# Kernel optimization log

Measured on AMD Instinct MI355X. Metric: run time of the kernel, lower is better.

The kernel has to match this reference:

```python
import jax, jax.numpy as jnp
import numpy as np

BINS = 10
GHM = 0.75
# edges = [0, 0.1, ..., 1.0], last edge nudged up as in the torch module
_EDGES = np.array([float(i) / BINS for i in range(BINS + 1)], dtype=np.float32)
_EDGES[-1] += 1e-6


def setup_inputs() -> dict:
    key = jax.random.key(0)
    k1, k2 = jax.random.split(key)
    shape = (32, 255, 80, 80)
    pred = jax.random.normal(k1, shape, dtype=jnp.float32)
    target = jax.random.randint(k2, shape, 0, 2).astype(jnp.float32)  # binary labels
    return {"pred": pred, "target": target}


def _ghmc_loss(pred, target):
    target = target.astype(jnp.float32)
    # gradient-norm proxy g = |sigmoid(pred) - target| in [0, 1]
    g = jnp.abs(jax.nn.sigmoid(pred) - target)
    total = float(np.prod(pred.shape))
    weights = jnp.zeros_like(pred)
    # 10-bin histogram weighting; loop over fixed bins is fine (not a data dim).
    # Inclusive edges overlap at boundaries; later bins overwrite, as in torch.
    for i in range(BINS):
        inds = (g >= _EDGES[i]) & (g <= _EDGES[i + 1])
        num_in_bin = jnp.sum(inds)
        # wherever inds is True, num_in_bin >= 1; maximum(.,1) avoids 0-div
        val = GHM * total / jnp.maximum(num_in_bin, 1).astype(pred.dtype)
        weights = jnp.where(inds, val, weights)
    weights = weights / 10.0
    # stable BCE-with-logits: max(x,0) - x*t + log(1 + exp(-|x|))
    bce = jnp.maximum(pred, 0.0) - pred * target + jnp.log1p(jnp.exp(-jnp.abs(pred)))
    return jnp.mean(weights * bce)  # reduction='mean'


def reference(pred, target):
    return _ghmc_loss(pred, target)
```

## Files before the change

kernel.cpp:

```cpp
#include <hip/hip_runtime.h>

#define NBINS 10
#define BLOCK 256
#define NW (BLOCK / 64)
#define GRID_MAX 2048

__device__ __forceinline__ void process_elem(float x, float tv,
                                             unsigned G[9], unsigned U[9],
                                             float fs[NBINS]) {
    const float E[NBINS + 1] = {0.0f, 0.1f, 0.2f, 0.3f, 0.4f, 0.5f,
                                0.6f, 0.7f, 0.8f, 0.9f, 1.000001f};
    float u   = __uint_as_float(__float_as_uint(x) ^ (__float_as_uint(tv) << 8));
    float au  = fabsf(u);
    float e   = __expf(-au);
    float ope = 1.0f + e;
    float r   = __builtin_amdgcn_rcpf(ope);
    float g   = (u >= 0.0f) ? r : e * r;
    float bce = fmaxf(u, 0.0f) + 0.69314718055994531f * __log2f(ope);

    bool prev = true;
#pragma unroll
    for (int k = 1; k <= 9; ++k) {
        bool ge_k = (g >= E[k]);
        bool gt_k = (g >  E[k]);
        G[k - 1] += ge_k ? 1u : 0u;
        U[k - 1] += gt_k ? 1u : 0u;
        fs[k - 1] += (prev && !ge_k) ? bce : 0.0f;
        prev = ge_k;
    }
    fs[9] += prev ? bce : 0.0f;
}

__global__ __launch_bounds__(BLOCK) void ghmc_main(
    const float* __restrict__ pred, const float* __restrict__ target,
    unsigned int* __restrict__ ws_cnt, float* __restrict__ ws_sum,
    long long nvec8, long long ntot, int direct, float* __restrict__ out) {
    unsigned G[9], U[9];
    float fs[NBINS];
#pragma unroll
    for (int k = 0; k < 9; ++k) { G[k] = 0u; U[k] = 0u; }
#pragma unroll
    for (int k = 0; k < NBINS; ++k) fs[k] = 0.0f;
    unsigned nloc = 0;

    const long long stride = (long long)gridDim.x * BLOCK;
    const long long tid0   = (long long)blockIdx.x * BLOCK + threadIdx.x;

    const float4* p4 = (const float4*)pred;
    const float4* t4 = (const float4*)target;
    for (long long i = tid0; i < nvec8; i += stride) {
        float4 p0 = p4[2 * i];
        float4 p1 = p4[2 * i + 1];
        float4 t0 = t4[2 * i];
        float4 t1 = t4[2 * i + 1];
        process_elem(p0.x, t0.x, G, U, fs);
        process_elem(p0.y, t0.y, G, U, fs);
        process_elem(p0.z, t0.z, G, U, fs);
        process_elem(p0.w, t0.w, G, U, fs);
        process_elem(p1.x, t1.x, G, U, fs);
        process_elem(p1.y, t1.y, G, U, fs);
        process_elem(p1.z, t1.z, G, U, fs);
        process_elem(p1.w, t1.w, G, U, fs);
        nloc += 8;
    }
    {
        long long base = nvec8 << 3;
        long long rem  = ntot - base;
        if (tid0 < rem) {
            process_elem(pred[base + tid0], target[base + tid0], G, U, fs);
            nloc += 1;
        }
    }

    unsigned cnt[NBINS];
    cnt[0] = nloc - U[0];
#pragma unroll
    for (int j = 1; j <= 8; ++j) cnt[j] = G[j - 1] - U[j];
    cnt[9] = G[8];

#pragma unroll
    for (int k = 0; k < NBINS; ++k) {
        unsigned int c = cnt[k];
        float        s = fs[k];
#pragma unroll
        for (int off = 32; off > 0; off >>= 1) {
            c += __shfl_down(c, off, 64);
            s += __shfl_down(s, off, 64);
        }
        cnt[k] = c;
        fs[k]  = s;
    }

    __shared__ unsigned int scnt[NW][NBINS];
    __shared__ float        ssum[NW][NBINS];
    int lane = threadIdx.x & 63;
    int wid  = threadIdx.x >> 6;
    if (lane == 0) {
#pragma unroll
        for (int k = 0; k < NBINS; ++k) {
            scnt[wid][k] = cnt[k];
            ssum[wid][k] = fs[k];
        }
    }
    __syncthreads();
    if (threadIdx.x == 0) {
        if (direct) {
            double loss = 0.0;
#pragma unroll
            for (int k = 0; k < NBINS; ++k) {
                unsigned int c = 0;
                double       s = 0.0;
#pragma unroll
                for (int w = 0; w < NW; ++w) { c += scnt[w][k]; s += (double)ssum[w][k]; }
                loss += s / (double)(c > 0u ? c : 1u);
            }
            out[0] = (float)(0.075 * loss);
        } else {
#pragma unroll
            for (int k = 0; k < NBINS; ++k) {
                unsigned int c = 0;
                float        s = 0.0f;
#pragma unroll
                for (int w = 0; w < NW; ++w) { c += scnt[w][k]; s += ssum[w][k]; }
                ws_cnt[(long long)blockIdx.x * NBINS + k] = c;
                ws_sum[(long long)blockIdx.x * NBINS + k] = s;
            }
        }
    }
}

__global__ __launch_bounds__(256) void ghmc_final(
    const unsigned int* __restrict__ ws_cnt, const float* __restrict__ ws_sum,
    int nblocks, float* __restrict__ out) {
    unsigned long long c[NBINS] = {};
    double             s[NBINS] = {};
    for (int b = threadIdx.x; b < nblocks; b += 256) {
#pragma unroll
        for (int k = 0; k < NBINS; ++k) {
            c[k] += ws_cnt[b * NBINS + k];
            s[k] += (double)ws_sum[b * NBINS + k];
        }
    }
#pragma unroll
    for (int k = 0; k < NBINS; ++k) {
        unsigned long long cc = c[k];
        double             ss = s[k];
#pragma unroll
        for (int off = 32; off > 0; off >>= 1) {
            cc += __shfl_down(cc, off, 64);
            ss += __shfl_down(ss, off, 64);
        }
        c[k] = cc;
        s[k] = ss;
    }
    __shared__ unsigned long long sc[4][NBINS];
    __shared__ double             sd[4][NBINS];
    int lane = threadIdx.x & 63;
    int wid  = threadIdx.x >> 6;
    if (lane == 0) {
#pragma unroll
        for (int k = 0; k < NBINS; ++k) { sc[wid][k] = c[k]; sd[wid][k] = s[k]; }
    }
    __syncthreads();
    if (threadIdx.x == 0) {
        double loss = 0.0;
#pragma unroll
        for (int k = 0; k < NBINS; ++k) {
            unsigned long long cc = 0;
            double             ss = 0.0;
#pragma unroll
            for (int w = 0; w < 4; ++w) { cc += sc[w][k]; ss += sd[w][k]; }
            loss += ss / (double)(cc > 0 ? cc : 1ull);
        }
        out[0] = (float)(0.075 * loss);
    }
}

extern "C" void kernel_launch(void* const* d_in, const int* in_sizes, int n_in,
                              void* d_out, int out_size, void* d_ws, size_t ws_size,
                              hipStream_t stream) {
    const float* pred   = (const float*)d_in[0];
    const float* target = (const float*)d_in[1];
    float*       out    = (float*)d_out;
    long long n     = (long long)in_sizes[0];
    long long nvec8 = n >> 3;

    const size_t per_block = NBINS * (sizeof(unsigned int) + sizeof(float));
    long long g = (nvec8 + BLOCK - 1) / BLOCK;
    if (g > GRID_MAX) g = GRID_MAX;
    long long g_ws = (long long)(ws_size / per_block);
    if (g > g_ws) g = g_ws;

    if (g < 1) {
        ghmc_main<<<1, BLOCK, 0, stream>>>(pred, target, nullptr, nullptr,
                                           nvec8, n, 1, out);
        return;
    }

    unsigned int* ws_cnt = (unsigned int*)d_ws;
    float*        ws_sum = (float*)((char*)d_ws + (size_t)g * NBINS * sizeof(unsigned int));

    ghmc_main<<<(int)g, BLOCK, 0, stream>>>(pred, target, ws_cnt, ws_sum,
                                            nvec8, n, 0, out);
    ghmc_final<<<1, 256, 0, stream>>>(ws_cnt, ws_sum, (int)g, out);
}
```

Measured before the change: 444.0 us.

## Bin in logit space with cumulative sums and wave ballot counts

```diff
diff --git a/kernel.cpp b/kernel.cpp
--- a/kernel.cpp
+++ b/kernel.cpp
@@ -1,129 +1,119 @@
 #include <hip/hip_runtime.h>
 
-#define NBINS 10
 #define BLOCK 256
 #define NW (BLOCK / 64)
 #define GRID_MAX 2048
 
-__device__ __forceinline__ void process_elem(float x, float tv,
-                                             unsigned G[9], unsigned U[9],
-                                             float fs[NBINS]) {
-    const float E[NBINS + 1] = {0.0f, 0.1f, 0.2f, 0.3f, 0.4f, 0.5f,
-                                0.6f, 0.7f, 0.8f, 0.9f, 1.000001f};
-    float u   = __uint_as_float(__float_as_uint(x) ^ (__float_as_uint(tv) << 8));
-    float au  = fabsf(u);
-    float e   = __expf(-au);
+__device__ __forceinline__ void process_u(float u, float a[10], unsigned G[10]) {
+    const float L[10] = {0.0f,
+        -2.1972245607794f, -1.3862943424934f, -0.8472978036209f,
+        -0.4054650832729f,  0.0f,              0.4054652074492f,
+         0.8472978036209f,  1.3862944356257f,  2.1972243124267f};
+    float e   = __expf(-fabsf(u));
     float ope = 1.0f + e;
-    float r   = __builtin_amdgcn_rcpf(ope);
-    float g   = (u >= 0.0f) ? r : e * r;
-    float bce = fmaxf(u, 0.0f) + 0.69314718055994531f * __log2f(ope);
-
-    bool prev = true;
+    float bce = fmaxf(u, 0.0f) + 0.693147180559945f * __log2f(ope);
+    a[0] += bce;
 #pragma unroll
     for (int k = 1; k <= 9; ++k) {
-        bool ge_k = (g >= E[k]);
-        bool gt_k = (g >  E[k]);
-        G[k - 1] += ge_k ? 1u : 0u;
-        U[k - 1] += gt_k ? 1u : 0u;
-        fs[k - 1] += (prev && !ge_k) ? bce : 0.0f;
-        prev = ge_k;
-    }
-    fs[9] += prev ? bce : 0.0f;
+        bool m = (u >= L[k]);
+        a[k] += m ? bce : 0.0f;
+        G[k] += (unsigned)__popcll(__ballot(m));
+    }
+}
+
+__device__ __forceinline__ float make_u(float x, float tv) {
+    return __uint_as_float(__float_as_uint(x) ^ (__float_as_uint(tv) << 8));
 }
 
 __global__ __launch_bounds__(BLOCK) void ghmc_main(
     const float* __restrict__ pred, const float* __restrict__ target,
     unsigned int* __restrict__ ws_cnt, float* __restrict__ ws_sum,
     long long nvec8, long long ntot, int direct, float* __restrict__ out) {
-    unsigned G[9], U[9];
-    float fs[NBINS];
-#pragma unroll
-    for (int k = 0; k < 9; ++k) { G[k] = 0u; U[k] = 0u; }
-#pragma unroll
-    for (int k = 0; k < NBINS; ++k) fs[k] = 0.0f;
-    unsigned nloc = 0;
+    float    a[10];
+    unsigned G[10];
+#pragma unroll
+    for (int k = 0; k < 10; ++k) { a[k] = 0.0f; G[k] = 0u; }
 
     const long long stride = (long long)gridDim.x * BLOCK;
     const long long tid0   = (long long)blockIdx.x * BLOCK + threadIdx.x;
 
+    const long long nvec8f = nvec8 & ~63LL;
     const float4* p4 = (const float4*)pred;
     const float4* t4 = (const float4*)target;
-    for (long long i = tid0; i < nvec8; i += stride) {
+    for (long long i = tid0; i < nvec8f; i += stride) {
         float4 p0 = p4[2 * i];
         float4 p1 = p4[2 * i + 1];
         float4 t0 = t4[2 * i];
         float4 t1 = t4[2 * i + 1];
-        process_elem(p0.x, t0.x, G, U, fs);
-        process_elem(p0.y, t0.y, G, U, fs);
-        process_elem(p0.z, t0.z, G, U, fs);
-        process_elem(p0.w, t0.w, G, U, fs);
-        process_elem(p1.x, t1.x, G, U, fs);
-        process_elem(p1.y, t1.y, G, U, fs);
-        process_elem(p1.z, t1.z, G, U, fs);
-        process_elem(p1.w, t1.w, G, U, fs);
-        nloc += 8;
-    }
-    {
-        long long base = nvec8 << 3;
+        process_u(make_u(p0.x, t0.x), a, G);
+        process_u(make_u(p0.y, t0.y), a, G);
+        process_u(make_u(p0.z, t0.z), a, G);
+        process_u(make_u(p0.w, t0.w), a, G);
+        process_u(make_u(p1.x, t1.x), a, G);
+        process_u(make_u(p1.y, t1.y), a, G);
+        process_u(make_u(p1.z, t1.z), a, G);
+        process_u(make_u(p1.w, t1.w), a, G);
+    }
+    if (blockIdx.x == 0) {
+        long long base = nvec8f << 3;
         long long rem  = ntot - base;
-        if (tid0 < rem) {
-            process_elem(pred[base + tid0], target[base + tid0], G, U, fs);
-            nloc += 1;
-        }
-    }
-
-    unsigned cnt[NBINS];
-    cnt[0] = nloc - U[0];
-#pragma unroll
-    for (int j = 1; j <= 8; ++j) cnt[j] = G[j - 1] - U[j];
-    cnt[9] = G[8];
-
-#pragma unroll
-    for (int k = 0; k < NBINS; ++k) {
-        unsigned int c = cnt[k];
-        float        s = fs[k];
-#pragma unroll
-        for (int off = 32; off > 0; off >>= 1) {
-            c += __shfl_down(c, off, 64);
-            s += __shfl_down(s, off, 64);
-        }
-        cnt[k] = c;
-        fs[k]  = s;
-    }
-
-    __shared__ unsigned int scnt[NW][NBINS];
-    __shared__ float        ssum[NW][NBINS];
+        int niter = (int)((rem + BLOCK - 1) / BLOCK);
+        for (int it = 0; it < niter; ++it) {
+            long long p = base + (long long)it * BLOCK + threadIdx.x;
+            bool v = (p < ntot);
+            long long pc = v ? p : 0;
+            float x  = pred[pc];
+            float tv = target[pc];
+            float u  = v ? make_u(x, tv) : -1e30f;
+            process_u(u, a, G);
+        }
+    }
+
+#pragma unroll
+    for (int k = 0; k < 10; ++k) {
+        float s = a[k];
+#pragma unroll
+        for (int off = 32; off > 0; off >>= 1) s += __shfl_down(s, off, 64);
+        a[k] = s;
+    }
+
+    __shared__ unsigned sG[NW][10];
+    __shared__ float    sA[NW][10];
     int lane = threadIdx.x & 63;
     int wid  = threadIdx.x >> 6;
     if (lane == 0) {
 #pragma unroll
-        for (int k = 0; k < NBINS; ++k) {
-            scnt[wid][k] = cnt[k];
-            ssum[wid][k] = fs[k];
-        }
+        for (int k = 0; k < 10; ++k) { sG[wid][k] = G[k]; sA[wid][k] = a[k]; }
     }
     __syncthreads();
     if (threadIdx.x == 0) {
+        unsigned gg[10];
+        float    aa[10];
+#pragma unroll
+        for (int k = 0; k < 10; ++k) {
+            unsigned c = 0; float s = 0.0f;
+#pragma unroll
+            for (int w = 0; w < NW; ++w) { c += sG[w][k]; s += sA[w][k]; }
+            gg[k] = c; aa[k] = s;
+        }
         if (direct) {
             double loss = 0.0;
 #pragma unroll
-            for (int k = 0; k < NBINS; ++k) {
-                unsigned int c = 0;
-                double       s = 0.0;
-#pragma unroll
-                for (int w = 0; w < NW; ++w) { c += scnt[w][k]; s += (double)ssum[w][k]; }
-                loss += s / (double)(c > 0u ? c : 1u);
+            for (int j = 0; j < 10; ++j) {
+                long long n = (j == 0) ? (long long)ntot - (long long)gg[1]
+                            : (j == 9) ? (long long)gg[9]
+                                       : (long long)gg[j] - (long long)gg[j + 1];
+                double S = (j == 0) ? (double)aa[0] - (double)aa[1]
+                         : (j == 9) ? (double)aa[9]
+                                    : (double)aa[j] - (double)aa[j + 1];
+                loss += S / (double)(n > 0 ? n : 1);
             }
             out[0] = (float)(0.075 * loss);
         } else {
 #pragma unroll
-            for (int k = 0; k < NBINS; ++k) {
-                unsigned int c = 0;
-                float        s = 0.0f;
-#pragma unroll
-                for (int w = 0; w < NW; ++w) { c += scnt[w][k]; s += ssum[w][k]; }
-                ws_cnt[(long long)blockIdx.x * NBINS + k] = c;
-                ws_sum[(long long)blockIdx.x * NBINS + k] = s;
+            for (int k = 0; k < 10; ++k) {
+                ws_cnt[(long long)blockIdx.x * 10 + k] = gg[k];
+                ws_sum[(long long)blockIdx.x * 10 + k] = aa[k];
             }
         }
     }
@@ -131,18 +121,18 @@
 
 __global__ __launch_bounds__(256) void ghmc_final(
     const unsigned int* __restrict__ ws_cnt, const float* __restrict__ ws_sum,
-    int nblocks, float* __restrict__ out) {
-    unsigned long long c[NBINS] = {};
-    double             s[NBINS] = {};
+    int nblocks, long long ntot, float* __restrict__ out) {
+    unsigned long long c[10] = {};
+    double             s[10] = {};
     for (int b = threadIdx.x; b < nblocks; b += 256) {
 #pragma unroll
-        for (int k = 0; k < NBINS; ++k) {
-            c[k] += ws_cnt[b * NBINS + k];
-            s[k] += (double)ws_sum[b * NBINS + k];
-        }
-    }
-#pragma unroll
-    for (int k = 0; k < NBINS; ++k) {
+        for (int k = 0; k < 10; ++k) {
+            c[k] += ws_cnt[b * 10 + k];
+            s[k] += (double)ws_sum[b * 10 + k];
+        }
+    }
+#pragma unroll
+    for (int k = 0; k < 10; ++k) {
         unsigned long long cc = c[k];
         double             ss = s[k];
 #pragma unroll
@@ -153,24 +143,33 @@
         c[k] = cc;
         s[k] = ss;
     }
-    __shared__ unsigned long long sc[4][NBINS];
-    __shared__ double             sd[4][NBINS];
+    __shared__ unsigned long long sc[4][10];
+    __shared__ double             sd[4][10];
     int lane = threadIdx.x & 63;
     int wid  = threadIdx.x >> 6;
     if (lane == 0) {
 #pragma unroll
-        for (int k = 0; k < NBINS; ++k) { sc[wid][k] = c[k]; sd[wid][k] = s[k]; }
+        for (int k = 0; k < 10; ++k) { sc[wid][k] = c[k]; sd[wid][k] = s[k]; }
     }
     __syncthreads();
     if (threadIdx.x == 0) {
+        unsigned long long gg[11];
+        double             aa[11];
+#pragma unroll
+        for (int k = 0; k < 10; ++k) {
+            unsigned long long cc = 0; double ss = 0.0;
+#pragma unroll
+            for (int w = 0; w < 4; ++w) { cc += sc[w][k]; ss += sd[w][k]; }
+            gg[k] = cc; aa[k] = ss;
+        }
+        gg[10] = 0ull; aa[10] = 0.0;
+        gg[0]  = (unsigned long long)ntot;
         double loss = 0.0;
 #pragma unroll
-        for (int k = 0; k < NBINS; ++k) {
-            unsigned long long cc = 0;
-            double             ss = 0.0;
-#pragma unroll
-            for (int w = 0; w < 4; ++w) { cc += sc[w][k]; ss += sd[w][k]; }
-            loss += ss / (double)(cc > 0 ? cc : 1ull);
+        for (int j = 0; j < 10; ++j) {
+            long long n = (long long)gg[j] - (long long)gg[j + 1];
+            double    S = aa[j] - aa[j + 1];
+            loss += S / (double)(n > 0 ? n : 1);
         }
         out[0] = (float)(0.075 * loss);
     }
@@ -185,7 +184,7 @@
     long long n     = (long long)in_sizes[0];
     long long nvec8 = n >> 3;
 
-    const size_t per_block = NBINS * (sizeof(unsigned int) + sizeof(float));
+    const size_t per_block = 10 * (sizeof(unsigned int) + sizeof(float));
     long long g = (nvec8 + BLOCK - 1) / BLOCK;
     if (g > GRID_MAX) g = GRID_MAX;
     long long g_ws = (long long)(ws_size / per_block);
@@ -198,9 +197,9 @@
     }
 
     unsigned int* ws_cnt = (unsigned int*)d_ws;
-    float*        ws_sum = (float*)((char*)d_ws + (size_t)g * NBINS * sizeof(unsigned int));
+    float*        ws_sum = (float*)((char*)d_ws + (size_t)g * 10 * sizeof(unsigned int));
 
     ghmc_main<<<(int)g, BLOCK, 0, stream>>>(pred, target, ws_cnt, ws_sum,
                                             nvec8, n, 0, out);
-    ghmc_final<<<1, 256, 0, stream>>>(ws_cnt, ws_sum, (int)g, out);
-}
+    ghmc_final<<<1, 256, 0, stream>>>(ws_cnt, ws_sum, (int)g, n, out);
+}
```

After: 416.0 us. 6.3% less time.
